# Performance work log

Hardware: AMD Instinct MI355X
Metric: run time of the kernel (lower is better)

## Reference

```python
import jax, jax.numpy as jnp
import numpy as np

N_EVENT = 100000
N_TRACE = 20000
E_EE = 1000000
E_ET = 500000
E_TE = 500000
D = 128          # embedding_dim == hidden_dim
OUT = 64         # output_dim
L = 3            # num_layers
NTYPES_EDGES = 3 # edge types
B = 64           # graphs per batch


def setup_inputs() -> dict:
    key = jax.random.key(0)
    ks = jax.random.split(key, 16)
    s = 1.0 / np.sqrt(D)
    inp = {
        "event_ids": jnp.arange(N_EVENT, dtype=jnp.int64 if jax.config.jax_enable_x64 else jnp.int32),
        "trace_ids": jnp.arange(N_TRACE, dtype=jnp.int64 if jax.config.jax_enable_x64 else jnp.int32),
        "e2e_src": jax.random.randint(ks[0], (E_EE,), 0, N_EVENT),
        "e2e_dst": jax.random.randint(ks[1], (E_EE,), 0, N_EVENT),
        "e2t_src": jax.random.randint(ks[2], (E_ET,), 0, N_EVENT),
        "e2t_dst": jax.random.randint(ks[3], (E_ET,), 0, N_TRACE),
        "t2e_src": jax.random.randint(ks[4], (E_TE,), 0, N_TRACE),
        "t2e_dst": jax.random.randint(ks[5], (E_TE,), 0, N_EVENT),
        "event_batch": jnp.sort(jax.random.randint(ks[6], (N_EVENT,), 0, B)),
        "trace_batch": jnp.sort(jax.random.randint(ks[7], (N_TRACE,), 0, B)),
        # learned parameters
        "emb_event": jax.random.normal(ks[8], (N_EVENT, D), jnp.float32),
        "emb_trace": jax.random.normal(ks[9], (N_TRACE, D), jnp.float32),
        # per-layer, per-edge-type SAGEConv weights: lin_l (neighbor, with bias), lin_r (root, no bias)
        "Wl": jax.random.normal(ks[10], (L, NTYPES_EDGES, D, D), jnp.float32) * s,
        "bl": jnp.zeros((L, NTYPES_EDGES, D), jnp.float32),
        "Wr": jax.random.normal(ks[11], (L, NTYPES_EDGES, D, D), jnp.float32) * s,
        # output MLP head
        "W1": jax.random.normal(ks[12], (D, D), jnp.float32) * s,
        "b1": jnp.zeros((D,), jnp.float32),
        "W2": jax.random.normal(ks[13], (OUT, D), jnp.float32) * s,
        "b2": jnp.zeros((OUT,), jnp.float32),
    }
    return inp


def reference(event_ids, trace_ids, e2e_src, e2e_dst, e2t_src, e2t_dst,
              t2e_src, t2e_dst, event_batch, trace_batch,
              emb_event, emb_trace, Wl, bl, Wr, W1, b1, W2, b2):
    def seg_mean(x_src, src, dst, n_dst):
        # mean-aggregate source features onto destination nodes (SAGEConv default aggr)
        s = jax.ops.segment_sum(x_src[src], dst, num_segments=n_dst)
        c = jax.ops.segment_sum(jnp.ones(dst.shape, x_src.dtype), dst, num_segments=n_dst)
        return s / jnp.maximum(c, 1.0)[:, None]

    # per-node-type embedding lookup
    x = {"event": emb_event[event_ids], "trace": emb_trace[trace_ids]}
    n = {"event": event_ids.shape[0], "trace": trace_ids.shape[0]}
    # edge types: (src_type, dst_type, src_idx, dst_idx), conv index matches Wl/bl/Wr axis 1
    edges = [
        ("event", "event", e2e_src, e2e_dst),
        ("event", "trace", e2t_src, e2t_dst),
        ("trace", "event", t2e_src, t2e_dst),
    ]
    n_layers = Wl.shape[0]
    for l in range(n_layers):
        new = {k: jnp.zeros((n[k], Wl.shape[-2]), x[k].dtype) for k in x}
        for i, (st, dt, s_idx, d_idx) in enumerate(edges):
            m = seg_mean(x[st], s_idx, d_idx, n[dt])
            # SAGEConv: lin_l(mean neighbors) + lin_r(root); HeteroConv aggr='sum' across edge types
            new[dt] = new[dt] + m @ Wl[l, i].T + bl[l, i] + x[dt] @ Wr[l, i].T
        x = new
    # global_add_pool per node type, then stack+sum over node types
    pooled = (jax.ops.segment_sum(x["event"], event_batch, num_segments=B)
              + jax.ops.segment_sum(x["trace"], trace_batch, num_segments=B))
    h = jax.nn.relu(pooled @ W1.T + b1)
    return h @ W2.T + b2
```

## Files before the change

kernel.cpp:

```cpp
#include <hip/hip_runtime.h>
#include <hip/hip_bf16.h>


#define D 128
#define NB 64
#define OUTD 64
#define NLAY 3
#define EPB 4096
#define BSH2 9

typedef __bf16 bf16;
typedef __bf16 bf16x4 __attribute__((ext_vector_type(4)));
typedef __bf16 bf16x8 __attribute__((ext_vector_type(8)));
typedef float  f32x16 __attribute__((ext_vector_type(16)));

#define LOAD16_TO_LDS(gp, lp) \
    __builtin_amdgcn_global_load_lds((const __attribute__((address_space(1))) void*)(gp), \
                                     (__attribute__((address_space(3))) void*)(lp), 16, 0, 0)

__global__ void gather_all(const float* __restrict__ embE, const int* __restrict__ idsE,
                           bf16* __restrict__ xE, int nE,
                           const float* __restrict__ embT, const int* __restrict__ idsT,
                           bf16* __restrict__ xT, int nT) {
    int idx = blockIdx.x * blockDim.x + threadIdx.x;
    const float* emb; const int* ids; bf16* x;
    int tE = nE * 32;
    if (idx < tE) { emb = embE; ids = idsE; x = xE; }
    else {
        idx -= tE;
        if (idx >= nT * 32) return;
        emb = embT; ids = idsT; x = xT;
    }
    int r = idx >> 5, v = idx & 31;
    float4 f = ((const float4*)(emb + (size_t)ids[r] * D))[v];
    bf16x4 o;
    o[0] = (bf16)f.x; o[1] = (bf16)f.y; o[2] = (bf16)f.z; o[3] = (bf16)f.w;
    ((bf16x4*)(x + (size_t)r * D))[v] = o;
}

__global__ void bkt_hist_all(const int* __restrict__ dEE, int nEE, int nbkEE, int nblkEE,
                             int* __restrict__ cntEE,
                             const int* __restrict__ dET, int nET, int nbkET, int nblkET,
                             int* __restrict__ cntET,
                             const int* __restrict__ dTE, int nTE, int nbkTE, int nblkTE,
                             int* __restrict__ cntTE) {
    __shared__ int h[256];
    int b = blockIdx.x;
    const int* dst; int E, nbk, nblk, lb; int* cnt;
    if (b < nblkEE) { dst = dEE; E = nEE; nbk = nbkEE; nblk = nblkEE; cnt = cntEE; lb = b; }
    else if (b < nblkEE + nblkET) { dst = dET; E = nET; nbk = nbkET; nblk = nblkET; cnt = cntET; lb = b - nblkEE; }
    else { dst = dTE; E = nTE; nbk = nbkTE; nblk = nblkTE; cnt = cntTE; lb = b - nblkEE - nblkET; }
    h[threadIdx.x] = 0;
    __syncthreads();
    int e0 = lb * EPB, e1 = min(e0 + EPB, E);
    for (int e = e0 + threadIdx.x; e < e1; e += 256) atomicAdd(&h[dst[e] >> BSH2], 1);
    __syncthreads();
    for (int k = threadIdx.x; k < nbk; k += 256) cnt[k * nblk + lb] = h[k];
}

__global__ void scan_p1_all(const int* __restrict__ dA, int* __restrict__ oA, int* __restrict__ sA, int nA,
                            const int* __restrict__ dB, int* __restrict__ oB, int* __restrict__ sB, int nB,
                            const int* __restrict__ dC, int* __restrict__ oC, int* __restrict__ sC, int nC) {
    int nbA = (nA + 1023) >> 10, nbB = (nB + 1023) >> 10;
    int b = blockIdx.x;
    const int* deg; int* off; int* bsum; int n; int lb;
    if (b < nbA) { deg = dA; off = oA; bsum = sA; n = nA; lb = b; }
    else if (b < nbA + nbB) { deg = dB; off = oB; bsum = sB; n = nB; lb = b - nbA; }
    else { deg = dC; off = oC; bsum = sC; n = nC; lb = b - nbA - nbB; }
    __shared__ int s[256];
    int t = threadIdx.x;
    int base = lb * 1024 + t * 4;
    int v[4];
    #pragma unroll
    for (int i = 0; i < 4; ++i) v[i] = (base + i < n) ? deg[base + i] : 0;
    int tot = v[0] + v[1] + v[2] + v[3];
    s[t] = tot;
    __syncthreads();
    for (int st = 1; st < 256; st <<= 1) {
        int x = (t >= st) ? s[t - st] : 0;
        __syncthreads();
        s[t] += x;
        __syncthreads();
    }
    int run = s[t] - tot;
    #pragma unroll
    for (int i = 0; i < 4; ++i) {
        if (base + i < n) off[base + i] = run;
        run += v[i];
    }
    if (t == 255) bsum[lb] = s[255];
}

__global__ void scan_p2_all(int* __restrict__ sA, int nbA,
                            int* __restrict__ sB, int nbB,
                            int* __restrict__ sC, int nbC) {
    int* bsum; int nb;
    if (blockIdx.x == 0) { bsum = sA; nb = nbA; }
    else if (blockIdx.x == 1) { bsum = sB; nb = nbB; }
    else { bsum = sC; nb = nbC; }
    __shared__ int s[256];
    int t = threadIdx.x;
    int v = (t < nb) ? bsum[t] : 0;
    s[t] = v;
    __syncthreads();
    for (int st = 1; st < 256; st <<= 1) {
        int x = (t >= st) ? s[t - st] : 0;
        __syncthreads();
        s[t] += x;
        __syncthreads();
    }
    if (t < nb) bsum[t] = s[t] - v;
    if (t == 0) bsum[nb] = s[255];
}

__global__ void scan_p3_all(int* __restrict__ oA, const int* __restrict__ sA, int nA,
                            int* __restrict__ oB, const int* __restrict__ sB, int nB,
                            int* __restrict__ oC, const int* __restrict__ sC, int nC) {
    int cbA = (nA + 255) >> 8, cbB = (nB + 255) >> 8;
    int b = blockIdx.x;
    int* off; const int* bsum; int n; int lb;
    if (b < cbA) { off = oA; bsum = sA; n = nA; lb = b; }
    else if (b < cbA + cbB) { off = oB; bsum = sB; n = nB; lb = b - cbA; }
    else { off = oC; bsum = sC; n = nC; lb = b - cbA - cbB; }
    int i = lb * 256 + threadIdx.x;
    if (i < n) off[i] += bsum[i >> 10];
    if (i == 0) off[n] = bsum[(n + 1023) >> 10];
}

__global__ void bkt_scatter_all(const int* __restrict__ sEE, const int* __restrict__ dEE,
                                int nEE, int nbkEE, int nblkEE, const int* __restrict__ SEE,
                                int2* __restrict__ ebEE,
                                const int* __restrict__ sET, const int* __restrict__ dET,
                                int nET, int nbkET, int nblkET, const int* __restrict__ SET,
                                int2* __restrict__ ebET,
                                const int* __restrict__ sTE, const int* __restrict__ dTE,
                                int nTE, int nbkTE, int nblkTE, const int* __restrict__ STE,
                                int2* __restrict__ ebTE) {
    __shared__ int cu[256];
    int b = blockIdx.x;
    const int* src; const int* dst; const int* S; int2* eb; int E, nbk, nblk, lb;
    if (b < nblkEE) { src = sEE; dst = dEE; S = SEE; eb = ebEE; E = nEE; nbk = nbkEE; nblk = nblkEE; lb = b; }
    else if (b < nblkEE + nblkET) { src = sET; dst = dET; S = SET; eb = ebET; E = nET; nbk = nbkET; nblk = nblkET; lb = b - nblkEE; }
    else { src = sTE; dst = dTE; S = STE; eb = ebTE; E = nTE; nbk = nbkTE; nblk = nblkTE; lb = b - nblkEE - nblkET; }
    for (int k = threadIdx.x; k < nbk; k += 256) cu[k] = S[k * nblk + lb];
    __syncthreads();
    int e0 = lb * EPB, e1 = min(e0 + EPB, E);
    for (int e = e0 + threadIdx.x; e < e1; e += 256) {
        int s = src[e], d = dst[e];
        int p = atomicAdd(&cu[d >> BSH2], 1);
        eb[p] = make_int2(s, d);
    }
}

__global__ void csr_build_all(const int2* __restrict__ ebEE, const int* __restrict__ SEE,
                              int nbkEE, int nblkEE, int ndEE,
                              int* __restrict__ offEE, int* __restrict__ adjEE,
                              const int2* __restrict__ ebET, const int* __restrict__ SET,
                              int nbkET, int nblkET, int ndET,
                              int* __restrict__ offET, int* __restrict__ adjET,
                              const int2* __restrict__ ebTE, const int* __restrict__ STE,
                              int nbkTE, int nblkTE, int ndTE,
                              int* __restrict__ offTE, int* __restrict__ adjTE) {
    __shared__ int h[512];
    __shared__ int ps[256];
    __shared__ int cc[512];
    int b = blockIdx.x;
    const int2* eb; const int* S; int nbk, nblk, ndst, k; int* off; int* adj;
    if (b < nbkEE) { eb = ebEE; S = SEE; nbk = nbkEE; nblk = nblkEE; ndst = ndEE; off = offEE; adj = adjEE; k = b; }
    else if (b < nbkEE + nbkET) { eb = ebET; S = SET; nbk = nbkET; nblk = nblkET; ndst = ndET; off = offET; adj = adjET; k = b - nbkEE; }
    else { eb = ebTE; S = STE; nbk = nbkTE; nblk = nblkTE; ndst = ndTE; off = offTE; adj = adjTE; k = b - nbkEE - nbkET; }
    int base = S[k * nblk];
    int end  = (k == nbk - 1) ? S[nbk * nblk] : S[(k + 1) * nblk];
    int d0 = k << BSH2;
    int t = threadIdx.x;
    h[t] = 0; h[t + 256] = 0;
    __syncthreads();
    for (int j = base + t; j < end; j += 256) atomicAdd(&h[eb[j].y - d0], 1);
    __syncthreads();
    int a0 = h[2 * t], a1 = h[2 * t + 1];
    ps[t] = a0 + a1;
    __syncthreads();
    for (int st = 1; st < 256; st <<= 1) {
        int x = (t >= st) ? ps[t - st] : 0;
        __syncthreads();
        ps[t] += x;
        __syncthreads();
    }
    int pe = ps[t] - (a0 + a1);
    int o0 = base + pe, o1 = base + pe + a0;
    cc[2 * t] = o0; cc[2 * t + 1] = o1;
    int nd = min(512, ndst - d0);
    if (2 * t < nd) off[d0 + 2 * t] = o0;
    if (2 * t + 1 < nd) off[d0 + 2 * t + 1] = o1;
    if (t == 0 && k == nbk - 1) off[ndst] = end;
    __syncthreads();
    for (int j = base + t; j < end; j += 256) {
        int2 e = eb[j];
        int p = atomicAdd(&cc[e.y - d0], 1);
        adj[p] = e.x;
    }
}

__global__ void agg_all(const bf16* __restrict__ xE, const bf16* __restrict__ xT,
                        const int* __restrict__ offEE, const int* __restrict__ adjEE,
                        const int* __restrict__ offTE, const int* __restrict__ adjTE,
                        const int* __restrict__ offET, const int* __restrict__ adjET,
                        bf16* __restrict__ mEE, bf16* __restrict__ mTE, bf16* __restrict__ mET,
                        int nE, int nT) {
    int gw = (blockIdx.x * blockDim.x + threadIdx.x) >> 6;
    int lane = threadIdx.x & 63;
    int qE = (nE + 3) >> 2, qT = (nT + 3) >> 2;
    const bf16* xsrc; const int* off; const int* adj; bf16* out; int ndst;
    if (gw < qE) { xsrc = xE; off = offEE; adj = adjEE; out = mEE; ndst = nE; }
    else if (gw < 2 * qE) { gw -= qE; xsrc = xT; off = offTE; adj = adjTE; out = mTE; ndst = nE; }
    else {
        gw -= 2 * qE;
        if (gw >= qT) return;
        xsrc = xE; off = offET; adj = adjET; out = mET; ndst = nT;
    }
    int sub = lane >> 4;
    int sl  = lane & 15;
    int row = gw * 4 + sub;
    if (row >= ndst) row = ndst - 1;
    int s0 = off[row], s1 = off[row + 1];
    float a[8] = {};
    int j = s0;
    for (; j + 8 <= s1; j += 8) {
        int ii[8];
        #pragma unroll
        for (int u = 0; u < 8; ++u) ii[u] = adj[j + u];
        bf16x8 v[8];
        #pragma unroll
        for (int u = 0; u < 8; ++u) v[u] = ((const bf16x8*)(xsrc + (size_t)ii[u] * D))[sl];
        #pragma unroll
        for (int u = 0; u < 8; ++u)
            #pragma unroll
            for (int e = 0; e < 8; ++e) a[e] += (float)v[u][e];
    }
    for (; j + 4 <= s1; j += 4) {
        int i0 = adj[j], i1 = adj[j + 1], i2 = adj[j + 2], i3 = adj[j + 3];
        bf16x8 v0 = ((const bf16x8*)(xsrc + (size_t)i0 * D))[sl];
        bf16x8 v1 = ((const bf16x8*)(xsrc + (size_t)i1 * D))[sl];
        bf16x8 v2 = ((const bf16x8*)(xsrc + (size_t)i2 * D))[sl];
        bf16x8 v3 = ((const bf16x8*)(xsrc + (size_t)i3 * D))[sl];
        #pragma unroll
        for (int e = 0; e < 8; ++e)
            a[e] += (float)v0[e] + (float)v1[e] + (float)v2[e] + (float)v3[e];
    }
    for (; j < s1; ++j) {
        int i0 = adj[j];
        bf16x8 v0 = ((const bf16x8*)(xsrc + (size_t)i0 * D))[sl];
        #pragma unroll
        for (int e = 0; e < 8; ++e) a[e] += (float)v0[e];
    }
    float inv = 1.0f / fmaxf((float)(s1 - s0), 1.0f);
    bf16x8 o;
    #pragma unroll
    for (int e = 0; e < 8; ++e) o[e] = (bf16)(a[e] * inv);
    ((bf16x8*)(out + (size_t)row * D))[sl] = o;
}

__global__ void prep_weights_packed(const float* __restrict__ Wl, const float* __restrict__ Wr,
                                    bf16* __restrict__ wbuf) {
    int idx = blockIdx.x * blockDim.x + threadIdx.x;
    if (idx >= NLAY * 5 * 2048) return;
    int l = idx / (5 * 2048);
    int rem = idx - l * 5 * 2048;
    int mat = rem >> 11;
    int q = rem & 2047;
    int lane = q & 63, t = (q >> 6) & 7, w = q >> 9;
    int r = w * 32 + (lane & 31);
    int c = t * 16 + (lane >> 5) * 8;
    size_t l3 = (size_t)l * 3;
    const float* s0;
    const float* s1 = nullptr;
    switch (mat) {
        case 0: s0 = Wl + (l3 + 0) * D * D; break;
        case 1: s0 = Wl + (l3 + 2) * D * D; break;
        case 2: s0 = Wr + (l3 + 0) * D * D; s1 = Wr + (l3 + 2) * D * D; break;
        case 3: s0 = Wl + (l3 + 1) * D * D; break;
        default: s0 = Wr + (l3 + 1) * D * D; break;
    }
    bf16x8 hi, lo;
    #pragma unroll
    for (int e = 0; e < 8; ++e) {
        float v = s0[r * D + c + e];
        if (s1) v += s1[r * D + c + e];
        bf16 h = (bf16)v;
        hi[e] = h;
        lo[e] = (bf16)(v - (float)h);
    }
    bf16* base = wbuf + (size_t)l * 10 * D * D;
    ((bf16x8*)(base + (size_t)(2 * mat) * D * D))[q] = hi;
    ((bf16x8*)(base + (size_t)(2 * mat + 1) * D * D))[q] = lo;
}

__global__ void prep_bias(const float* __restrict__ bl, float* __restrict__ bbuf) {
    int idx = blockIdx.x * blockDim.x + threadIdx.x;
    if (idx >= NLAY * D) return;
    int l = idx >> 7, o = idx & (D - 1);
    bbuf[l * 2 * D + o]     = bl[(size_t)(l * 3 + 0) * D + o] + bl[(size_t)(l * 3 + 2) * D + o];
    bbuf[l * 2 * D + D + o] = bl[(size_t)(l * 3 + 1) * D + o];
}

__device__ __forceinline__ void gemm_body(const bf16* A0, const bf16* A1, const bf16* A2,
                                          const bf16* Wp, const float* bias, bf16* out,
                                          int M, int nm, int row0, bf16* As) {
    int tid = threadIdx.x;
    int wave = tid >> 6, lane = tid & 63;
    int m = lane & 31, half = lane >> 5;

    f32x16 acc[2];
    #pragma unroll
    for (int rt = 0; rt < 2; ++rt)
        #pragma unroll
        for (int i = 0; i < 16; ++i) acc[rt][i] = 0.f;

    const bf16* Aptr[3] = {A0, A1, A2};
    #pragma unroll
    for (int s = 0; s < 3; ++s) {
        if (s >= nm) break;
        if (s) __syncthreads();
        const bf16* Amat = Aptr[s];
        #pragma unroll
        for (int p = 0; p < 4; ++p) {
            int si = p * 256 + tid;
            int r = si >> 4, u = si & 15;
            int gr = row0 + r; if (gr >= M) gr = M - 1;
            int gc = (u ^ (r & 15)) * 8;
            LOAD16_TO_LDS(Amat + (size_t)gr * D + gc, As + (size_t)(p * 4 + wave) * 512);
        }
        const bf16* wph = Wp + (size_t)(2 * s) * D * D + ((size_t)wave * 512 + lane) * 8;
        const bf16* wpl = wph + D * D;
        bf16x8 bh_c  = *(const bf16x8*)(wph);
        bf16x8 blo_c = *(const bf16x8*)(wpl);
        __syncthreads();

        #pragma unroll 1
        for (int t = 0; t < 8; ++t) {
            bf16x8 bh_n, blo_n;
            if (t < 7) {
                bh_n  = *(const bf16x8*)(wph + (t + 1) * 512);
                blo_n = *(const bf16x8*)(wpl + (t + 1) * 512);
            }
            bf16x8 af[2];
            #pragma unroll
            for (int rt = 0; rt < 2; ++rt) {
                int r = rt * 32 + m;
                int c = t * 2 + half;
                af[rt] = *(const bf16x8*)(As + ((size_t)r * 16 + (c ^ (r & 15))) * 8);
            }
            acc[0] = __builtin_amdgcn_mfma_f32_32x32x16_bf16(af[0], bh_c,  acc[0], 0, 0, 0);
            acc[1] = __builtin_amdgcn_mfma_f32_32x32x16_bf16(af[1], bh_c,  acc[1], 0, 0, 0);
            acc[0] = __builtin_amdgcn_mfma_f32_32x32x16_bf16(af[0], blo_c, acc[0], 0, 0, 0);
            acc[1] = __builtin_amdgcn_mfma_f32_32x32x16_bf16(af[1], blo_c, acc[1], 0, 0, 0);
            bh_c = bh_n; blo_c = blo_n;
        }
    }

    int col = wave * 32 + m;
    float bv = bias[col];
    #pragma unroll
    for (int rt = 0; rt < 2; ++rt) {
        #pragma unroll
        for (int r = 0; r < 16; ++r) {
            int row = row0 + rt * 32 + (r & 3) + 8 * (r >> 2) + 4 * half;
            if (row < M) out[(size_t)row * D + col] = (bf16)(acc[rt][r] + bv);
        }
    }
}

__global__ __launch_bounds__(256) void gemm_all(const bf16* __restrict__ eA0, const bf16* __restrict__ eA1,
                                                const bf16* __restrict__ eA2, const bf16* __restrict__ eW,
                                                const float* __restrict__ eB, bf16* __restrict__ eOut,
                                                int Me, int bE,
                                                const bf16* __restrict__ tA0, const bf16* __restrict__ tA1,
                                                const bf16* __restrict__ tW, const float* __restrict__ tB,
                                                bf16* __restrict__ tOut, int Mt) {
    __shared__ bf16 As[64 * 128];
    if ((int)blockIdx.x < bE)
        gemm_body(eA0, eA1, eA2, eW, eB, eOut, Me, 3, blockIdx.x * 64, As);
    else
        gemm_body(tA0, tA1, (const bf16*)nullptr, tW, tB, tOut, Mt, 2,
                  ((int)blockIdx.x - bE) * 64, As);
}

__global__ void pool_m_all(const bf16* __restrict__ m_ee, const bf16* __restrict__ m_te,
                           const bf16* __restrict__ xE, const bf16* __restrict__ m_et,
                           const bf16* __restrict__ xT,
                           const int* __restrict__ bEv, const int* __restrict__ bTr,
                           int nE, int nT, int pbE, int pbT,
                           float* __restrict__ pooled5, int* __restrict__ cntE,
                           int* __restrict__ cntT) {
    int c = threadIdx.x;
    int blk = blockIdx.x;
    const bf16* x; const int* batch; int n, r0, s;
    if (blk < 3 * pbE) {
        s = blk / pbE; int lb = blk - s * pbE;
        x = (s == 0) ? m_ee : (s == 1) ? m_te : xE;
        batch = bEv; n = nE; r0 = lb * 64;
    } else {
        int q = blk - 3 * pbE;
        s = 3 + q / pbT; int lb = q - (s - 3) * pbT;
        x = (s == 3) ? m_et : xT;
        batch = bTr; n = nT; r0 = lb * 64;
    }
    int r1 = min(r0 + 64, n);
    if (r0 >= r1) return;
    float* P = pooled5 + (size_t)s * NB * D;
    int* cnt = (s == 2) ? cntE : (s == 4) ? cntT : nullptr;
    int cur = batch[r0];
    float acc = 0.f;
    int run = 0;
    for (int r = r0; r < r1; ++r) {
        int b = batch[r];
        if (b != cur) {
            atomicAdd(&P[cur * D + c], acc);
            if (cnt && c == 0) atomicAdd(&cnt[cur], run);
            acc = 0.f; run = 0; cur = b;
        }
        acc += (float)x[(size_t)r * D + c];
        run++;
    }
    atomicAdd(&P[cur * D + c], acc);
    if (cnt && c == 0) atomicAdd(&cnt[cur], run);
}

__global__ void tail_kernel(const float* __restrict__ pooled5, const int* __restrict__ cntE,
                            const int* __restrict__ cntT,
                            const float* __restrict__ Wl, const float* __restrict__ Wr,
                            const float* __restrict__ bl,
                            const float* __restrict__ W1, const float* __restrict__ b1,
                            const float* __restrict__ W2, const float* __restrict__ b2,
                            float* __restrict__ out) {
    __shared__ float p5[5][D];
    __shared__ float hp[D];
    __shared__ float hh[D];
    int b = blockIdx.x, t = threadIdx.x;
    #pragma unroll
    for (int s = 0; s < 5; ++s) p5[s][t] = pooled5[(size_t)(s * NB + b) * D + t];
    __syncthreads();
    float ce = (float)cntE[b], ct = (float)cntT[b];
    float s = ce * (bl[6 * D + t] + bl[8 * D + t]) + ct * bl[7 * D + t];
    const float* w0  = Wl + (size_t)6 * D * D + (size_t)t * D;
    const float* w2  = Wl + (size_t)8 * D * D + (size_t)t * D;
    const float* wr0 = Wr + (size_t)6 * D * D + (size_t)t * D;
    const float* wr2 = Wr + (size_t)8 * D * D + (size_t)t * D;
    const float* w1m = Wl + (size_t)7 * D * D + (size_t)t * D;
    const float* wr1 = Wr + (size_t)7 * D * D + (size_t)t * D;
    #pragma unroll 4
    for (int k = 0; k < D; ++k)
        s += p5[0][k] * w0[k] + p5[1][k] * w2[k] + p5[2][k] * (wr0[k] + wr2[k])
           + p5[3][k] * w1m[k] + p5[4][k] * wr1[k];
    hp[t] = s;
    __syncthreads();
    float s1 = b1[t];
    const float* u = W1 + (size_t)t * D;
    #pragma unroll 4
    for (int k = 0; k < D; ++k) s1 += hp[k] * u[k];
    hh[t] = fmaxf(s1, 0.f);
    __syncthreads();
    if (t < OUTD) {
        float s2 = b2[t];
        const float* v = W2 + (size_t)t * D;
        #pragma unroll 4
        for (int k = 0; k < D; ++k) s2 += hh[k] * v[k];
        out[b * OUTD + t] = s2;
    }
}

extern "C" void kernel_launch(void* const* d_in, const int* in_sizes, int n_in,
                              void* d_out, int out_size, void* d_ws, size_t ws_size,
                              hipStream_t stream) {
    const int* event_ids   = (const int*)d_in[0];
    const int* trace_ids   = (const int*)d_in[1];
    const int* e2e_src     = (const int*)d_in[2];
    const int* e2e_dst     = (const int*)d_in[3];
    const int* e2t_src     = (const int*)d_in[4];
    const int* e2t_dst     = (const int*)d_in[5];
    const int* t2e_src     = (const int*)d_in[6];
    const int* t2e_dst     = (const int*)d_in[7];
    const int* event_batch = (const int*)d_in[8];
    const int* trace_batch = (const int*)d_in[9];
    const float* emb_event = (const float*)d_in[10];
    const float* emb_trace = (const float*)d_in[11];
    const float* Wl        = (const float*)d_in[12];
    const float* bl        = (const float*)d_in[13];
    const float* Wr        = (const float*)d_in[14];
    const float* W1        = (const float*)d_in[15];
    const float* b1        = (const float*)d_in[16];
    const float* W2        = (const float*)d_in[17];
    const float* b2        = (const float*)d_in[18];

    const int NE = in_sizes[0];
    const int NT = in_sizes[1];
    const int EE = in_sizes[2];
    const int ET = in_sizes[4];
    const int TE = in_sizes[6];

    const int nbkEE = (NE + 511) >> BSH2, nblkEE = (EE + EPB - 1) / EPB;
    const int nbkET = (NT + 511) >> BSH2, nblkET = (ET + EPB - 1) / EPB;
    const int nbkTE = (NE + 511) >> BSH2, nblkTE = (TE + EPB - 1) / EPB;
    const int cEE = nbkEE * nblkEE, cET = nbkET * nblkET, cTE = nbkTE * nblkTE;

    size_t cur = 0;
    auto alloc = [&](size_t bytes) -> void* {
        cur = (cur + 255) & ~(size_t)255;
        void* p = (char*)d_ws + cur;
        cur += bytes;
        return p;
    };
    bf16* x_event   = (bf16*)alloc((size_t)NE * D * 2);
    bf16* x_trace   = (bf16*)alloc((size_t)NT * D * 2);
    bf16* nx_event  = (bf16*)alloc((size_t)NE * D * 2);
    bf16* nx_trace  = (bf16*)alloc((size_t)NT * D * 2);
    bf16* m_ee      = (bf16*)alloc((size_t)NE * D * 2);
    bf16* m_te      = (bf16*)alloc((size_t)NE * D * 2);
    bf16* m_et      = (bf16*)alloc((size_t)NT * D * 2);
    bf16* wbuf      = (bf16*)alloc((size_t)NLAY * 10 * D * D * 2);
    float* bbuf     = (float*)alloc((size_t)NLAY * 2 * D * 4);
    size_t zInts = (size_t)5 * NB * D + 2 * NB;
    int* zbase  = (int*)alloc(zInts * 4);
    float* pooled5 = (float*)zbase;
    int* cntE = (int*)(pooled5 + 5 * NB * D);
    int* cntT = cntE + NB;
    int* off_ee = (int*)alloc((size_t)(NE + 1) * 4);
    int* adj_ee = (int*)alloc((size_t)EE * 4);
    int* off_et = (int*)alloc((size_t)(NT + 1) * 4);
    int* adj_et = (int*)alloc((size_t)ET * 4);
    int* off_te = (int*)alloc((size_t)(NE + 1) * 4);
    int* adj_te = (int*)alloc((size_t)TE * 4);
    int* cnt_ee = (int*)alloc((size_t)cEE * 4);
    int* S_ee   = (int*)alloc((size_t)(cEE + 1) * 4);
    int* cnt_et = (int*)alloc((size_t)cET * 4);
    int* S_et   = (int*)alloc((size_t)(cET + 1) * 4);
    int* cnt_te = (int*)alloc((size_t)cTE * 4);
    int* S_te   = (int*)alloc((size_t)(cTE + 1) * 4);
    int* bsum_ee = (int*)alloc(((size_t)(cEE + 1023) / 1024 + 1) * 4);
    int* bsum_et = (int*)alloc(((size_t)(cET + 1023) / 1024 + 1) * 4);
    int* bsum_te = (int*)alloc(((size_t)(cTE + 1023) / 1024 + 1) * 4);
    int2* eb_ee = (int2*)m_ee;
    int2* eb_et = (int2*)m_te;
    int2* eb_te = (int2*)m_et;
    (void)ws_size; (void)n_in; (void)out_size;

    hipMemsetAsync(zbase, 0, zInts * 4, stream);

    gather_all<<<((NE + NT) * 32 + 255) / 256, 256, 0, stream>>>(
        emb_event, event_ids, x_event, NE, emb_trace, trace_ids, x_trace, NT);

    prep_weights_packed<<<(NLAY * 5 * 2048 + 255) / 256, 256, 0, stream>>>(Wl, Wr, wbuf);
    prep_bias<<<(NLAY * D + 255) / 256, 256, 0, stream>>>(bl, bbuf);

    bkt_hist_all<<<nblkEE + nblkET + nblkTE, 256, 0, stream>>>(
        e2e_dst, EE, nbkEE, nblkEE, cnt_ee,
        e2t_dst, ET, nbkET, nblkET, cnt_et,
        t2e_dst, TE, nbkTE, nblkTE, cnt_te);
    const int nb1 = (cEE + 1023) >> 10, nb2 = (cET + 1023) >> 10, nb3 = (cTE + 1023) >> 10;
    scan_p1_all<<<nb1 + nb2 + nb3, 256, 0, stream>>>(
        cnt_ee, S_ee, bsum_ee, cEE, cnt_et, S_et, bsum_et, cET, cnt_te, S_te, bsum_te, cTE);
    scan_p2_all<<<3, 256, 0, stream>>>(bsum_ee, nb1, bsum_et, nb2, bsum_te, nb3);
    scan_p3_all<<<((cEE + 255) >> 8) + ((cET + 255) >> 8) + ((cTE + 255) >> 8), 256, 0, stream>>>(
        S_ee, bsum_ee, cEE, S_et, bsum_et, cET, S_te, bsum_te, cTE);
    bkt_scatter_all<<<nblkEE + nblkET + nblkTE, 256, 0, stream>>>(
        e2e_src, e2e_dst, EE, nbkEE, nblkEE, S_ee, eb_ee,
        e2t_src, e2t_dst, ET, nbkET, nblkET, S_et, eb_et,
        t2e_src, t2e_dst, TE, nbkTE, nblkTE, S_te, eb_te);
    csr_build_all<<<nbkEE + nbkET + nbkTE, 256, 0, stream>>>(
        eb_ee, S_ee, nbkEE, nblkEE, NE, off_ee, adj_ee,
        eb_et, S_et, nbkET, nblkET, NT, off_et, adj_et,
        eb_te, S_te, nbkTE, nblkTE, NE, off_te, adj_te);

    const int qE = (NE + 3) >> 2, qT = (NT + 3) >> 2;
    const int aggBlocks = (2 * qE + qT + 3) / 4;
    const int bE = (NE + 63) / 64, bT = (NT + 63) / 64;
    for (int l = 0; l < NLAY; ++l) {
        agg_all<<<aggBlocks, 256, 0, stream>>>(x_event, x_trace,
                                               off_ee, adj_ee, off_te, adj_te, off_et, adj_et,
                                               m_ee, m_te, m_et, NE, NT);
        if (l < NLAY - 1) {
            const bf16* wl_ev = wbuf + (size_t)l * 10 * D * D;
            const bf16* wl_tr = wl_ev + (size_t)6 * D * D;
            const float* be = bbuf + (size_t)l * 2 * D;
            const float* bt = be + D;
            gemm_all<<<bE + bT, 256, 0, stream>>>(m_ee, m_te, x_event, wl_ev, be, nx_event, NE, bE,
                                                  m_et, x_trace, wl_tr, bt, nx_trace, NT);
            bf16* t;
            t = x_event; x_event = nx_event; nx_event = t;
            t = x_trace; x_trace = nx_trace; nx_trace = t;
        }
    }

    const int pbE = (NE + 63) / 64, pbT = (NT + 63) / 64;
    pool_m_all<<<3 * pbE + 2 * pbT, D, 0, stream>>>(m_ee, m_te, x_event, m_et, x_trace,
                                                    event_batch, trace_batch, NE, NT, pbE, pbT,
                                                    pooled5, cntE, cntT);
    tail_kernel<<<NB, D, 0, stream>>>(pooled5, cntE, cntT, Wl, Wr, bl,
                                      W1, b1, W2, b2, (float*)d_out);
}
```

Baseline: 602.3 us.

## Pool by precomputed batch segment bounds and fuse scan passes

```diff
diff --git a/kernel.cpp b/kernel.cpp
--- a/kernel.cpp
+++ b/kernel.cpp
@@ -8,6 +8,7 @@
 #define NLAY 3
 #define EPB 4096
 #define BSH2 9
+#define PSPLIT 4
 
 typedef __bf16 bf16;
 typedef __bf16 bf16x4 __attribute__((ext_vector_type(4)));
@@ -21,8 +22,26 @@
 __global__ void gather_all(const float* __restrict__ embE, const int* __restrict__ idsE,
                            bf16* __restrict__ xE, int nE,
                            const float* __restrict__ embT, const int* __restrict__ idsT,
-                           bf16* __restrict__ xT, int nT) {
-    int idx = blockIdx.x * blockDim.x + threadIdx.x;
+                           bf16* __restrict__ xT, int nT,
+                           const int* __restrict__ bEv, const int* __restrict__ bTr,
+                           int* __restrict__ boundsE, int* __restrict__ boundsT,
+                           int nGather) {
+    int b = blockIdx.x;
+    if (b == nGather) {
+        int t = threadIdx.x;
+        if (t <= NB) {
+            int lo = 0, hi = nE;
+            while (lo < hi) { int mid = (lo + hi) >> 1; if (bEv[mid] < t) lo = mid + 1; else hi = mid; }
+            boundsE[t] = lo;
+        } else if (t <= 2 * NB + 1) {
+            int v = t - NB - 1;
+            int lo = 0, hi = nT;
+            while (lo < hi) { int mid = (lo + hi) >> 1; if (bTr[mid] < v) lo = mid + 1; else hi = mid; }
+            boundsT[v] = lo;
+        }
+        return;
+    }
+    int idx = b * 256 + threadIdx.x;
     const float* emb; const int* ids; bf16* x;
     int tE = nE * 32;
     if (idx < tE) { emb = embE; ids = idsE; x = xE; }
@@ -91,40 +110,33 @@
     if (t == 255) bsum[lb] = s[255];
 }
 
-__global__ void scan_p2_all(int* __restrict__ sA, int nbA,
-                            int* __restrict__ sB, int nbB,
-                            int* __restrict__ sC, int nbC) {
-    int* bsum; int nb;
-    if (blockIdx.x == 0) { bsum = sA; nb = nbA; }
-    else if (blockIdx.x == 1) { bsum = sB; nb = nbB; }
-    else { bsum = sC; nb = nbC; }
-    __shared__ int s[256];
-    int t = threadIdx.x;
-    int v = (t < nb) ? bsum[t] : 0;
-    s[t] = v;
-    __syncthreads();
-    for (int st = 1; st < 256; st <<= 1) {
-        int x = (t >= st) ? s[t - st] : 0;
-        __syncthreads();
-        s[t] += x;
-        __syncthreads();
-    }
-    if (t < nb) bsum[t] = s[t] - v;
-    if (t == 0) bsum[nb] = s[255];
-}
-
-__global__ void scan_p3_all(int* __restrict__ oA, const int* __restrict__ sA, int nA,
-                            int* __restrict__ oB, const int* __restrict__ sB, int nB,
-                            int* __restrict__ oC, const int* __restrict__ sC, int nC) {
+__global__ void scan_p23_all(int* __restrict__ oA, const int* __restrict__ sA, int nA,
+                             int* __restrict__ oB, const int* __restrict__ sB, int nB,
+                             int* __restrict__ oC, const int* __restrict__ sC, int nC) {
     int cbA = (nA + 255) >> 8, cbB = (nB + 255) >> 8;
     int b = blockIdx.x;
     int* off; const int* bsum; int n; int lb;
     if (b < cbA) { off = oA; bsum = sA; n = nA; lb = b; }
     else if (b < cbA + cbB) { off = oB; bsum = sB; n = nB; lb = b - cbA; }
     else { off = oC; bsum = sC; n = nC; lb = b - cbA - cbB; }
-    int i = lb * 256 + threadIdx.x;
-    if (i < n) off[i] += bsum[i >> 10];
-    if (i == 0) off[n] = bsum[(n + 1023) >> 10];
+    __shared__ int s[256];
+    __shared__ int ex[256];
+    int nb = (n + 1023) >> 10;
+    int t = threadIdx.x;
+    int v = (t < nb) ? bsum[t] : 0;
+    s[t] = v;
+    __syncthreads();
+    for (int st = 1; st < 256; st <<= 1) {
+        int x = (t >= st) ? s[t - st] : 0;
+        __syncthreads();
+        s[t] += x;
+        __syncthreads();
+    }
+    ex[t] = s[t] - v;
+    __syncthreads();
+    int i = lb * 256 + t;
+    if (i < n) off[i] += ex[i >> 10];
+    if (i == 0) off[n] = s[nb - 1];
 }
 
 __global__ void bkt_scatter_all(const int* __restrict__ sEE, const int* __restrict__ dEE,
@@ -385,49 +397,53 @@
                   ((int)blockIdx.x - bE) * 64, As);
 }
 
-__global__ void pool_m_all(const bf16* __restrict__ m_ee, const bf16* __restrict__ m_te,
-                           const bf16* __restrict__ xE, const bf16* __restrict__ m_et,
-                           const bf16* __restrict__ xT,
-                           const int* __restrict__ bEv, const int* __restrict__ bTr,
-                           int nE, int nT, int pbE, int pbT,
-                           float* __restrict__ pooled5, int* __restrict__ cntE,
-                           int* __restrict__ cntT) {
+__global__ void pool_group_all(const bf16* __restrict__ m_ee, const bf16* __restrict__ m_te,
+                               const bf16* __restrict__ xE, const bf16* __restrict__ m_et,
+                               const bf16* __restrict__ xT,
+                               const int* __restrict__ boundsE, const int* __restrict__ boundsT,
+                               float* __restrict__ pooled5) {
+    __shared__ float red[16][D];
+    int blk = blockIdx.x;
+    int s = blk / (NB * PSPLIT);
+    int rem = blk - s * NB * PSPLIT;
+    int b = rem / PSPLIT;
+    int j = rem - b * PSPLIT;
+    const bf16* x; const int* bounds;
+    switch (s) {
+        case 0: x = m_ee; bounds = boundsE; break;
+        case 1: x = m_te; bounds = boundsE; break;
+        case 2: x = xE;   bounds = boundsE; break;
+        case 3: x = m_et; bounds = boundsT; break;
+        default: x = xT;  bounds = boundsT; break;
+    }
+    int start = bounds[b], end = bounds[b + 1];
+    int len = end - start;
+    if (len <= 0) return;
+    int r0 = start + (int)(((long long)len * j) / PSPLIT);
+    int r1 = start + (int)(((long long)len * (j + 1)) / PSPLIT);
+    if (r0 >= r1) return;
+    int slot = threadIdx.x >> 4;
+    int ch   = threadIdx.x & 15;
+    float a[8] = {};
+    for (int r = r0 + slot; r < r1; r += 16) {
+        bf16x8 v = ((const bf16x8*)(x + (size_t)r * D))[ch];
+        #pragma unroll
+        for (int e = 0; e < 8; ++e) a[e] += (float)v[e];
+    }
+    #pragma unroll
+    for (int e = 0; e < 8; ++e) red[slot][ch * 8 + e] = a[e];
+    __syncthreads();
     int c = threadIdx.x;
-    int blk = blockIdx.x;
-    const bf16* x; const int* batch; int n, r0, s;
-    if (blk < 3 * pbE) {
-        s = blk / pbE; int lb = blk - s * pbE;
-        x = (s == 0) ? m_ee : (s == 1) ? m_te : xE;
-        batch = bEv; n = nE; r0 = lb * 64;
-    } else {
-        int q = blk - 3 * pbE;
-        s = 3 + q / pbT; int lb = q - (s - 3) * pbT;
-        x = (s == 3) ? m_et : xT;
-        batch = bTr; n = nT; r0 = lb * 64;
-    }
-    int r1 = min(r0 + 64, n);
-    if (r0 >= r1) return;
-    float* P = pooled5 + (size_t)s * NB * D;
-    int* cnt = (s == 2) ? cntE : (s == 4) ? cntT : nullptr;
-    int cur = batch[r0];
-    float acc = 0.f;
-    int run = 0;
-    for (int r = r0; r < r1; ++r) {
-        int b = batch[r];
-        if (b != cur) {
-            atomicAdd(&P[cur * D + c], acc);
-            if (cnt && c == 0) atomicAdd(&cnt[cur], run);
-            acc = 0.f; run = 0; cur = b;
-        }
-        acc += (float)x[(size_t)r * D + c];
-        run++;
-    }
-    atomicAdd(&P[cur * D + c], acc);
-    if (cnt && c == 0) atomicAdd(&cnt[cur], run);
-}
-
-__global__ void tail_kernel(const float* __restrict__ pooled5, const int* __restrict__ cntE,
-                            const int* __restrict__ cntT,
+    if (c < D) {
+        float ssum = 0.f;
+        #pragma unroll
+        for (int k = 0; k < 16; ++k) ssum += red[k][c];
+        atomicAdd(&pooled5[(size_t)s * NB * D + b * D + c], ssum);
+    }
+}
+
+__global__ void tail_kernel(const float* __restrict__ pooled5,
+                            const int* __restrict__ boundsE, const int* __restrict__ boundsT,
                             const float* __restrict__ Wl, const float* __restrict__ Wr,
                             const float* __restrict__ bl,
                             const float* __restrict__ W1, const float* __restrict__ b1,
@@ -440,7 +456,8 @@
     #pragma unroll
     for (int s = 0; s < 5; ++s) p5[s][t] = pooled5[(size_t)(s * NB + b) * D + t];
     __syncthreads();
-    float ce = (float)cntE[b], ct = (float)cntT[b];
+    float ce = (float)(boundsE[b + 1] - boundsE[b]);
+    float ct = (float)(boundsT[b + 1] - boundsT[b]);
     float s = ce * (bl[6 * D + t] + bl[8 * D + t]) + ct * bl[7 * D + t];
     const float* w0  = Wl + (size_t)6 * D * D + (size_t)t * D;
     const float* w2  = Wl + (size_t)8 * D * D + (size_t)t * D;
@@ -519,11 +536,11 @@
     bf16* m_et      = (bf16*)alloc((size_t)NT * D * 2);
     bf16* wbuf      = (bf16*)alloc((size_t)NLAY * 10 * D * D * 2);
     float* bbuf     = (float*)alloc((size_t)NLAY * 2 * D * 4);
-    size_t zInts = (size_t)5 * NB * D + 2 * NB;
+    size_t zInts = (size_t)5 * NB * D;
     int* zbase  = (int*)alloc(zInts * 4);
     float* pooled5 = (float*)zbase;
-    int* cntE = (int*)(pooled5 + 5 * NB * D);
-    int* cntT = cntE + NB;
+    int* boundsE = (int*)alloc((size_t)(NB + 1) * 4);
+    int* boundsT = (int*)alloc((size_t)(NB + 1) * 4);
     int* off_ee = (int*)alloc((size_t)(NE + 1) * 4);
     int* adj_ee = (int*)alloc((size_t)EE * 4);
     int* off_et = (int*)alloc((size_t)(NT + 1) * 4);
@@ -546,8 +563,10 @@
 
     hipMemsetAsync(zbase, 0, zInts * 4, stream);
 
-    gather_all<<<((NE + NT) * 32 + 255) / 256, 256, 0, stream>>>(
-        emb_event, event_ids, x_event, NE, emb_trace, trace_ids, x_trace, NT);
+    const int nGather = ((NE + NT) * 32 + 255) / 256;
+    gather_all<<<nGather + 1, 256, 0, stream>>>(
+        emb_event, event_ids, x_event, NE, emb_trace, trace_ids, x_trace, NT,
+        event_batch, trace_batch, boundsE, boundsT, nGather);
 
     prep_weights_packed<<<(NLAY * 5 * 2048 + 255) / 256, 256, 0, stream>>>(Wl, Wr, wbuf);
     prep_bias<<<(NLAY * D + 255) / 256, 256, 0, stream>>>(bl, bbuf);
@@ -559,8 +578,7 @@
     const int nb1 = (cEE + 1023) >> 10, nb2 = (cET + 1023) >> 10, nb3 = (cTE + 1023) >> 10;
     scan_p1_all<<<nb1 + nb2 + nb3, 256, 0, stream>>>(
         cnt_ee, S_ee, bsum_ee, cEE, cnt_et, S_et, bsum_et, cET, cnt_te, S_te, bsum_te, cTE);
-    scan_p2_all<<<3, 256, 0, stream>>>(bsum_ee, nb1, bsum_et, nb2, bsum_te, nb3);
-    scan_p3_all<<<((cEE + 255) >> 8) + ((cET + 255) >> 8) + ((cTE + 255) >> 8), 256, 0, stream>>>(
+    scan_p23_all<<<((cEE + 255) >> 8) + ((cET + 255) >> 8) + ((cTE + 255) >> 8), 256, 0, stream>>>(
         S_ee, bsum_ee, cEE, S_et, bsum_et, cET, S_te, bsum_te, cTE);
     bkt_scatter_all<<<nblkEE + nblkET + nblkTE, 256, 0, stream>>>(
         e2e_src, e2e_dst, EE, nbkEE, nblkEE, S_ee, eb_ee,
@@ -591,10 +609,8 @@
         }
     }
 
-    const int pbE = (NE + 63) / 64, pbT = (NT + 63) / 64;
-    pool_m_all<<<3 * pbE + 2 * pbT, D, 0, stream>>>(m_ee, m_te, x_event, m_et, x_trace,
-                                                    event_batch, trace_batch, NE, NT, pbE, pbT,
-                                                    pooled5, cntE, cntT);
-    tail_kernel<<<NB, D, 0, stream>>>(pooled5, cntE, cntT, Wl, Wr, bl,
+    pool_group_all<<<5 * NB * PSPLIT, 256, 0, stream>>>(m_ee, m_te, x_event, m_et, x_trace,
+                                                        boundsE, boundsT, pooled5);
+    tail_kernel<<<NB, D, 0, stream>>>(pooled5, boundsE, boundsT, Wl, Wr, bl,
                                       W1, b1, W2, b2, (float*)d_out);
 }
```

New measurement: 571.3 us. 1.05x faster.
